# Kernel optimization log

Measured on AMD Instinct MI355X. Metric: run time of the kernel, lower is better.

## Reference

```python
import jax, jax.numpy as jnp
import numpy as np

E, K = 8, 2            # num_experts, top_k
H, DFF = 1024, 2048    # embd_dim, d_ff
B, S = 4, 1024


def setup_inputs() -> dict:
    key = jax.random.key(0)
    ks = jax.random.split(key, 5)
    s_in = 1.0 / np.sqrt(H)
    s_ff = 1.0 / np.sqrt(DFF)
    return {
        "x": jax.random.normal(ks[0], (B, S, H), jnp.float32),
        "centroids": jax.random.normal(ks[1], (E, H), jnp.float32),
        # nn.Linear weights are [out, in]
        "gate_w": jax.random.normal(ks[2], (E, DFF, H), jnp.float32) * s_in,
        "up_w": jax.random.normal(ks[3], (E, DFF, H), jnp.float32) * s_in,
        "down_w": jax.random.normal(ks[4], (E, H, DFF), jnp.float32) * s_ff,
        "routing_bias": jnp.zeros((E,), jnp.float32),
    }


def reference(x, centroids, gate_w, up_w, down_w, routing_bias):
    Bb, Ss, Hh = x.shape
    xf = x.reshape(-1, Hh)  # [T, H]
    # sigmoid affinity router + (non-trainable) routing bias
    affinity = jax.nn.sigmoid(xf @ centroids.T)          # [T, E]
    topk_scores, topk_idx = jax.lax.top_k(affinity + routing_bias, K)  # [T, K]
    topk_w = jax.nn.softmax(topk_scores, axis=-1)        # [T, K]

    # Dense per-expert SwiGLU FFN on all tokens (same math as the
    # sort/gather grouped loop; selection happens in the gather below).
    g = jnp.einsum('th,efh->etf', xf, gate_w)            # [E, T, DFF]
    u = jnp.einsum('th,efh->etf', xf, up_w)              # [E, T, DFF]
    y = jnp.einsum('etf,ehf->eth', jax.nn.silu(g) * u, down_w)  # [E, T, H]

    yt = jnp.transpose(y, (1, 0, 2))                     # [T, E, H]
    sel = jnp.take_along_axis(yt, topk_idx[:, :, None], axis=1)  # [T, K, H]
    out_flat = jnp.sum(sel * topk_w[:, :, None], axis=1)  # [T, H]

    counts = jnp.bincount(topk_idx.ravel(), length=E)    # per-expert token counts
    return out_flat.reshape(Bb, Ss, Hh), counts
```

## Files before the change

### kernel.cpp

```cpp
#include <hip/hip_runtime.h>
#include <math.h>

constexpr int E = 8, H = 1024, DFF = 2048, T = 4096;
constexpr int TR = 8192;
constexpr int MAXJ = 72;

typedef __bf16 bf16x8 __attribute__((ext_vector_type(8)));
typedef __bf16 bf16x4 __attribute__((ext_vector_type(4)));
typedef float f32x4 __attribute__((ext_vector_type(4)));

__device__ __forceinline__ void gload16(const void* g, void* l) {
    __builtin_amdgcn_global_load_lds(
        (const __attribute__((address_space(1))) unsigned int*)g,
        (__attribute__((address_space(3))) unsigned int*)l, 16, 0, 0);
}

__global__ __launch_bounds__(256) void k1_affinity(
    const float* __restrict__ x, const float* __restrict__ cent,
    const float* __restrict__ bias,
    int* __restrict__ se, float* __restrict__ sw) {
    __shared__ float cs[E * H];
    int tid = threadIdx.x;
    for (int i = tid; i < E * H / 4; i += 256)
        ((float4*)cs)[i] = ((const float4*)cent)[i];
    __syncthreads();

    int wave = tid >> 6, lane = tid & 63;
    int t = blockIdx.x * 4 + wave;
    const float4* xr = (const float4*)(x + (size_t)t * H);
    float acc[E] = {};
    #pragma unroll
    for (int it = 0; it < 4; it++) {
        float4 xv = xr[lane + it * 64];
        #pragma unroll
        for (int e = 0; e < E; e++) {
            float4 cv = ((const float4*)(cs + e * H))[lane + it * 64];
            acc[e] = fmaf(xv.x, cv.x, acc[e]);
            acc[e] = fmaf(xv.y, cv.y, acc[e]);
            acc[e] = fmaf(xv.z, cv.z, acc[e]);
            acc[e] = fmaf(xv.w, cv.w, acc[e]);
        }
    }
    #pragma unroll
    for (int off = 32; off; off >>= 1)
        #pragma unroll
        for (int e = 0; e < E; e++) acc[e] += __shfl_down(acc[e], off);

    if (lane == 0) {
        float s[E];
        #pragma unroll
        for (int e = 0; e < E; e++)
            s[e] = 1.0f / (1.0f + expf(-acc[e])) + bias[e];
        int i0 = 0;
        for (int e = 1; e < E; e++) if (s[e] > s[i0]) i0 = e;
        int i1 = -1;
        for (int e = 0; e < E; e++) {
            if (e == i0) continue;
            if (i1 < 0 || s[e] > s[i1]) i1 = e;
        }
        float m = fmaxf(s[i0], s[i1]);
        float w0 = expf(s[i0] - m), w1 = expf(s[i1] - m);
        float inv = 1.0f / (w0 + w1);
        se[2 * t] = i0;     sw[2 * t] = w0 * inv;
        se[2 * t + 1] = i1; sw[2 * t + 1] = w1 * inv;
    }
}

__global__ __launch_bounds__(256) void k1b_partition(
    const int* __restrict__ se, int* __restrict__ token_list,
    int* __restrict__ sp, int* __restrict__ cnt) {
    int e = blockIdx.x;
    int tid = threadIdx.x;
    int wave = tid >> 6, lane = tid & 63;
    __shared__ int wsum[4];
    int running = 0;
    for (int c0 = 0; c0 < 2 * T; c0 += 256) {
        int i = c0 + tid;
        bool pred = (se[i] == e);
        unsigned long long mask = __ballot(pred);
        int pos_in_wave = __popcll(mask & ((1ull << lane) - 1ull));
        if (lane == 0) wsum[wave] = __popcll(mask);
        __syncthreads();
        int wbase = 0;
        for (int w2 = 0; w2 < wave; w2++) wbase += wsum[w2];
        int total = wsum[0] + wsum[1] + wsum[2] + wsum[3];
        if (pred) {
            int p = running + wbase + pos_in_wave;
            token_list[e * T + p] = i >> 1;
            sp[i] = p;
        }
        running += total;
        __syncthreads();
    }
    if (tid == 0) cnt[e] = running;
}

__global__ void k15_offsets(const int* __restrict__ cnt, int* __restrict__ off,
                            float* __restrict__ out_counts,
                            int* __restrict__ jobs, int* __restrict__ njobs) {
    if (threadIdx.x == 0) {
        int acc = 0, nj = 0;
        for (int e = 0; e < E; e++) {
            off[e] = acc; acc += cnt[e];
            int mts = (cnt[e] + 127) >> 7;
            for (int mt = 0; mt < mts; mt++) jobs[nj++] = e * 64 + mt;
        }
        njobs[0] = nj;
    }
    if (threadIdx.x < E) out_counts[threadIdx.x] = (float)cnt[threadIdx.x];
}

__global__ __launch_bounds__(256) void k_conv(const float* __restrict__ in,
                                              __bf16* __restrict__ out, int n4) {
    int i = blockIdx.x * 256 + threadIdx.x;
    if (i < n4) {
        float4 v = ((const float4*)in)[i];
        bf16x4 o = {(__bf16)v.x, (__bf16)v.y, (__bf16)v.z, (__bf16)v.w};
        ((bf16x4*)out)[i] = o;
    }
}

__global__ __launch_bounds__(256) void k_conv3(
    const float* __restrict__ gw, __bf16* __restrict__ gwb,
    const float* __restrict__ uw, __bf16* __restrict__ uwb,
    const float* __restrict__ x, __bf16* __restrict__ xb,
    int w4, int x4) {
    int i = blockIdx.x * 256 + threadIdx.x;
    const float* in; __bf16* out; int idx;
    if (i < w4) { in = gw; out = gwb; idx = i; }
    else if (i < 2 * w4) { in = uw; out = uwb; idx = i - w4; }
    else { idx = i - 2 * w4; if (idx >= x4) return; in = x; out = xb; }
    float4 v = ((const float4*)in)[idx];
    bf16x4 o = {(__bf16)v.x, (__bf16)v.y, (__bf16)v.z, (__bf16)v.w};
    ((bf16x4*)out)[idx] = o;
}

__global__ __launch_bounds__(256, 2) void k2_gateup(
    const __bf16* __restrict__ xb, const __bf16* __restrict__ gwb,
    const __bf16* __restrict__ uwb, const int* __restrict__ cnt,
    const int* __restrict__ off, const int* __restrict__ token_list,
    const int* __restrict__ jobs, const int* __restrict__ njobs,
    __bf16* __restrict__ h) {
    int jt = blockIdx.x >> 4, nt = blockIdx.x & 15;
    if (jt >= njobs[0]) return;
    int job = jobs[jt];
    int e = job >> 6, mt = job & 63;
    int Me = cnt[e], offe = off[e];

    __shared__ __bf16 As[128 * 64];
    __shared__ __bf16 Bg[128 * 64];
    __shared__ __bf16 Bu[128 * 64];

    int tid = threadIdx.x;
    int lane = tid & 63, w = tid >> 6;
    int wm = w >> 1, wn = w & 1;

    const __bf16* asrc[4];
    const __bf16 *bsg[4], *bsu[4];
    #pragma unroll
    for (int rr = 0; rr < 4; rr++) {
        int l = rr * 256 + tid;
        int row = l >> 3, sl = l & 7;
        int gr = mt * 128 + row; if (gr >= Me) gr = Me - 1;
        int tok = token_list[e * T + gr];
        asrc[rr] = xb + (size_t)tok * H + ((sl ^ (row & 7)) * 8);
        size_t base = ((size_t)e * DFF + nt * 128 + row) * H + ((sl ^ (row & 7)) * 8);
        bsg[rr] = gwb + base;
        bsu[rr] = uwb + base;
    }

    f32x4 accg[4][4] = {};
    f32x4 accu[4][4] = {};
    int kq = lane >> 4, m15 = lane & 15;

    for (int k0 = 0; k0 < H; k0 += 64) {
        #pragma unroll
        for (int rr = 0; rr < 4; rr++) {
            gload16(asrc[rr] + k0, &As[(rr * 256 + tid) * 8]);
            gload16(bsg[rr] + k0, &Bg[(rr * 256 + tid) * 8]);
            gload16(bsu[rr] + k0, &Bu[(rr * 256 + tid) * 8]);
        }
        __syncthreads();

        #pragma unroll
        for (int kc = 0; kc < 2; kc++) {
            bf16x8 af[4], gf[4], uf[4];
            #pragma unroll
            for (int i = 0; i < 4; i++) {
                int row = wm * 64 + i * 16 + m15;
                int sl = (kc * 4 + kq) ^ (row & 7);
                af[i] = *(const bf16x8*)&As[row * 64 + sl * 8];
            }
            #pragma unroll
            for (int j = 0; j < 4; j++) {
                int row = wn * 64 + j * 16 + m15;
                int sl = (kc * 4 + kq) ^ (row & 7);
                gf[j] = *(const bf16x8*)&Bg[row * 64 + sl * 8];
                uf[j] = *(const bf16x8*)&Bu[row * 64 + sl * 8];
            }
            #pragma unroll
            for (int i = 0; i < 4; i++)
                #pragma unroll
                for (int j = 0; j < 4; j++) {
                    accg[i][j] = __builtin_amdgcn_mfma_f32_16x16x32_bf16(af[i], gf[j], accg[i][j], 0, 0, 0);
                    accu[i][j] = __builtin_amdgcn_mfma_f32_16x16x32_bf16(af[i], uf[j], accu[i][j], 0, 0, 0);
                }
        }
        __syncthreads();
    }

    #pragma unroll
    for (int i = 0; i < 4; i++)
        #pragma unroll
        for (int j = 0; j < 4; j++) {
            int nloc = wn * 64 + j * 16 + m15;
            size_t c = (size_t)nt * 128 + nloc;
            #pragma unroll
            for (int p = 0; p < 4; p++) {
                int mloc = wm * 64 + i * 16 + kq * 4 + p;
                int mrow = mt * 128 + mloc;
                if (mrow < Me) {
                    float g = accg[i][j][p], u = accu[i][j][p];
                    float sig = 1.0f / (1.0f + __expf(-g));
                    h[(size_t)(offe + mrow) * DFF + c] = (__bf16)(g * sig * u);
                }
            }
        }
}

__global__ __launch_bounds__(512, 2) void k3_down(
    const __bf16* __restrict__ h, const __bf16* __restrict__ dwb,
    const int* __restrict__ cnt, const int* __restrict__ off,
    const int* __restrict__ jobs, const int* __restrict__ njobs,
    __bf16* __restrict__ y) {
    int jt = blockIdx.x >> 2, nt = blockIdx.x & 3;
    if (jt >= njobs[0]) return;
    int job = jobs[jt];
    int e = job >> 6, mt = job & 63;
    int Me = cnt[e], offe = off[e];

    __shared__ __bf16 As[128 * 64];
    __shared__ __bf16 Bs[256 * 64];

    int tid = threadIdx.x;
    int lane = tid & 63, w = tid >> 6;
    int wm = w >> 2, wn = w & 3;

    const __bf16* asrc[2];
    #pragma unroll
    for (int rr = 0; rr < 2; rr++) {
        int l = rr * 512 + tid;
        int row = l >> 3, sl = l & 7;
        int koff = (sl ^ (row & 7)) * 8;
        int gr = mt * 128 + row; if (gr >= Me) gr = Me - 1;
        asrc[rr] = h + (size_t)(offe + gr) * DFF + koff;
    }
    const __bf16* bsrc[4];
    #pragma unroll
    for (int rr = 0; rr < 4; rr++) {
        int l = rr * 512 + tid;
        int row = l >> 3, sl = l & 7;
        int koff = (sl ^ (row & 7)) * 8;
        bsrc[rr] = dwb + ((size_t)e * H + nt * 256 + row) * DFF + koff;
    }

    f32x4 acc[4][4] = {};
    int kq = lane >> 4, m15 = lane & 15;

    for (int k0 = 0; k0 < DFF; k0 += 64) {
        #pragma unroll
        for (int rr = 0; rr < 2; rr++)
            gload16(asrc[rr] + k0, &As[(rr * 512 + tid) * 8]);
        #pragma unroll
        for (int rr = 0; rr < 4; rr++)
            gload16(bsrc[rr] + k0, &Bs[(rr * 512 + tid) * 8]);
        __syncthreads();

        #pragma unroll
        for (int kc = 0; kc < 2; kc++) {
            bf16x8 af[4], bf[4];
            #pragma unroll
            for (int i = 0; i < 4; i++) {
                int row = wm * 64 + i * 16 + m15;
                int sl = (kc * 4 + kq) ^ (row & 7);
                af[i] = *(const bf16x8*)&As[row * 64 + sl * 8];
            }
            #pragma unroll
            for (int j = 0; j < 4; j++) {
                int row = wn * 64 + j * 16 + m15;
                int sl = (kc * 4 + kq) ^ (row & 7);
                bf[j] = *(const bf16x8*)&Bs[row * 64 + sl * 8];
            }
            #pragma unroll
            for (int i = 0; i < 4; i++)
                #pragma unroll
                for (int j = 0; j < 4; j++)
                    acc[i][j] = __builtin_amdgcn_mfma_f32_16x16x32_bf16(af[i], bf[j], acc[i][j], 0, 0, 0);
        }
        __syncthreads();
    }

    #pragma unroll
    for (int i = 0; i < 4; i++)
        #pragma unroll
        for (int j = 0; j < 4; j++) {
            int nglob = nt * 256 + wn * 64 + j * 16 + m15;
            #pragma unroll
            for (int p = 0; p < 4; p++) {
                int mloc = wm * 64 + i * 16 + kq * 4 + p;
                int mrow = mt * 128 + mloc;
                if (mrow < Me)
                    y[(size_t)(offe + mrow) * H + nglob] = (__bf16)acc[i][j][p];
            }
        }
}

__global__ __launch_bounds__(256) void k_gather(
    const __bf16* __restrict__ y, const int* __restrict__ se,
    const int* __restrict__ sp, const float* __restrict__ sw,
    const int* __restrict__ off, float* __restrict__ out) {
    int t = blockIdx.x;
    int r0 = off[se[2 * t]] + sp[2 * t];
    int r1 = off[se[2 * t + 1]] + sp[2 * t + 1];
    float w0 = sw[2 * t], w1 = sw[2 * t + 1];
    const bf16x4* y0 = (const bf16x4*)(y + (size_t)r0 * H);
    const bf16x4* y1 = (const bf16x4*)(y + (size_t)r1 * H);
    float4* o = (float4*)(out + (size_t)t * H);
    int c = threadIdx.x;
    bf16x4 a = y0[c], b = y1[c];
    float4 v;
    v.x = w0 * (float)a[0] + w1 * (float)b[0];
    v.y = w0 * (float)a[1] + w1 * (float)b[1];
    v.z = w0 * (float)a[2] + w1 * (float)b[2];
    v.w = w0 * (float)a[3] + w1 * (float)b[3];
    o[c] = v;
}

extern "C" void kernel_launch(void* const* d_in, const int* in_sizes, int n_in,
                              void* d_out, int out_size, void* d_ws, size_t ws_size,
                              hipStream_t stream) {
    const float* x    = (const float*)d_in[0];
    const float* cent = (const float*)d_in[1];
    const float* gw   = (const float*)d_in[2];
    const float* uw   = (const float*)d_in[3];
    const float* dw   = (const float*)d_in[4];
    const float* bias = (const float*)d_in[5];
    float* out = (float*)d_out;

    char* ws = (char*)d_ws;
    int*   cnt        = (int*)(ws + 0);
    int*   off        = (int*)(ws + 64);
    int*   se         = (int*)(ws + 128);
    int*   sp         = (int*)(ws + 128 + 32768);
    float* sw         = (float*)(ws + 128 + 65536);
    int*   token_list = (int*)(ws + 128 + 98304);
    int*   jobs       = (int*)(ws + 229504);
    int*   njobs      = (int*)(ws + 229824);
    const size_t MB = 1u << 20;
    __bf16* gwb = (__bf16*)(ws + 1 * MB);
    __bf16* uwb = (__bf16*)(ws + 1 * MB + 33554432);
    __bf16* dwb = gwb;
    __bf16* y   = uwb;
    __bf16* xb  = (__bf16*)(ws + 1 * MB + 67108864);
    __bf16* h   = (__bf16*)(ws + 1 * MB + 75497472);

    const int W4 = E * DFF * H / 4;
    const int X4 = T * H / 4;
    const int C3 = 2 * W4 + X4;

    k_conv3<<<(C3 + 255) / 256, 256, 0, stream>>>(gw, gwb, uw, uwb, x, xb, W4, X4);
    k1_affinity<<<T / 4, 256, 0, stream>>>(x, cent, bias, se, sw);
    k1b_partition<<<E, 256, 0, stream>>>(se, token_list, sp, cnt);
    k15_offsets<<<1, 64, 0, stream>>>(cnt, off, out + (size_t)T * H, jobs, njobs);
    k2_gateup<<<MAXJ * 16, 256, 0, stream>>>(xb, gwb, uwb, cnt, off, token_list, jobs, njobs, h);
    k_conv<<<(W4 + 255) / 256, 256, 0, stream>>>(dw, dwb, W4);
    k3_down<<<MAXJ * 4, 512, 0, stream>>>(h, dwb, cnt, off, jobs, njobs, y);
    k_gather<<<T, 256, 0, stream>>>(y, se, sp, sw, off, out);
}
```

Before: 389.4 us.

## Fuse weighted combine into down-proj via atomics and fold x conversion into router

The down-projection epilogue now scales each row by its routing weight and atomically adds it into the zero-initialised fp32 output, which removes the intermediate y buffer and the separate gather kernel. The bf16 conversion of x moves into the affinity kernel, and the partition kernel stores per-row weights instead of slot positions. Launch-bound occupancy hints are raised for both GEMMs. In exchange it adds a memset of the output, scattered fp32 atomics that make the summation order nondeterministic, and possible register pressure from the higher occupancy targets.

```diff
diff --git a/kernel.cpp b/kernel.cpp
--- a/kernel.cpp
+++ b/kernel.cpp
@@ -18,7 +18,7 @@
 __global__ __launch_bounds__(256) void k1_affinity(
     const float* __restrict__ x, const float* __restrict__ cent,
     const float* __restrict__ bias,
-    int* __restrict__ se, float* __restrict__ sw) {
+    int* __restrict__ se, float* __restrict__ sw, __bf16* __restrict__ xb) {
     __shared__ float cs[E * H];
     int tid = threadIdx.x;
     for (int i = tid; i < E * H / 4; i += 256)
@@ -28,10 +28,13 @@
     int wave = tid >> 6, lane = tid & 63;
     int t = blockIdx.x * 4 + wave;
     const float4* xr = (const float4*)(x + (size_t)t * H);
+    bf16x4* xw = (bf16x4*)(xb + (size_t)t * H);
     float acc[E] = {};
     #pragma unroll
     for (int it = 0; it < 4; it++) {
         float4 xv = xr[lane + it * 64];
+        bf16x4 o = {(__bf16)xv.x, (__bf16)xv.y, (__bf16)xv.z, (__bf16)xv.w};
+        xw[lane + it * 64] = o;
         #pragma unroll
         for (int e = 0; e < E; e++) {
             float4 cv = ((const float4*)(cs + e * H))[lane + it * 64];
@@ -67,8 +70,9 @@
 }
 
 __global__ __launch_bounds__(256) void k1b_partition(
-    const int* __restrict__ se, int* __restrict__ token_list,
-    int* __restrict__ sp, int* __restrict__ cnt) {
+    const int* __restrict__ se, const float* __restrict__ sw,
+    int* __restrict__ token_list, float* __restrict__ roww,
+    int* __restrict__ cnt) {
     int e = blockIdx.x;
     int tid = threadIdx.x;
     int wave = tid >> 6, lane = tid & 63;
@@ -87,7 +91,7 @@
         if (pred) {
             int p = running + wbase + pos_in_wave;
             token_list[e * T + p] = i >> 1;
-            sp[i] = p;
+            roww[e * T + p] = sw[i];
         }
         running += total;
         __syncthreads();
@@ -120,22 +124,19 @@
     }
 }
 
-__global__ __launch_bounds__(256) void k_conv3(
+__global__ __launch_bounds__(256) void k_conv2(
     const float* __restrict__ gw, __bf16* __restrict__ gwb,
-    const float* __restrict__ uw, __bf16* __restrict__ uwb,
-    const float* __restrict__ x, __bf16* __restrict__ xb,
-    int w4, int x4) {
+    const float* __restrict__ uw, __bf16* __restrict__ uwb, int w4) {
     int i = blockIdx.x * 256 + threadIdx.x;
     const float* in; __bf16* out; int idx;
     if (i < w4) { in = gw; out = gwb; idx = i; }
-    else if (i < 2 * w4) { in = uw; out = uwb; idx = i - w4; }
-    else { idx = i - 2 * w4; if (idx >= x4) return; in = x; out = xb; }
+    else { idx = i - w4; if (idx >= w4) return; in = uw; out = uwb; }
     float4 v = ((const float4*)in)[idx];
     bf16x4 o = {(__bf16)v.x, (__bf16)v.y, (__bf16)v.z, (__bf16)v.w};
     ((bf16x4*)out)[idx] = o;
 }
 
-__global__ __launch_bounds__(256, 2) void k2_gateup(
+__global__ __launch_bounds__(256, 3) void k2_gateup(
     const __bf16* __restrict__ xb, const __bf16* __restrict__ gwb,
     const __bf16* __restrict__ uwb, const int* __restrict__ cnt,
     const int* __restrict__ off, const int* __restrict__ token_list,
@@ -228,11 +229,12 @@
         }
 }
 
-__global__ __launch_bounds__(512, 2) void k3_down(
+__global__ __launch_bounds__(512, 4) void k3_down(
     const __bf16* __restrict__ h, const __bf16* __restrict__ dwb,
     const int* __restrict__ cnt, const int* __restrict__ off,
+    const int* __restrict__ token_list, const float* __restrict__ roww,
     const int* __restrict__ jobs, const int* __restrict__ njobs,
-    __bf16* __restrict__ y) {
+    float* __restrict__ out) {
     int jt = blockIdx.x >> 2, nt = blockIdx.x & 3;
     if (jt >= njobs[0]) return;
     int job = jobs[jt];
@@ -301,39 +303,22 @@
     }
 
     #pragma unroll
-    for (int i = 0; i < 4; i++)
-        #pragma unroll
-        for (int j = 0; j < 4; j++) {
-            int nglob = nt * 256 + wn * 64 + j * 16 + m15;
-            #pragma unroll
-            for (int p = 0; p < 4; p++) {
-                int mloc = wm * 64 + i * 16 + kq * 4 + p;
-                int mrow = mt * 128 + mloc;
-                if (mrow < Me)
-                    y[(size_t)(offe + mrow) * H + nglob] = (__bf16)acc[i][j][p];
-            }
-        }
-}
-
-__global__ __launch_bounds__(256) void k_gather(
-    const __bf16* __restrict__ y, const int* __restrict__ se,
-    const int* __restrict__ sp, const float* __restrict__ sw,
-    const int* __restrict__ off, float* __restrict__ out) {
-    int t = blockIdx.x;
-    int r0 = off[se[2 * t]] + sp[2 * t];
-    int r1 = off[se[2 * t + 1]] + sp[2 * t + 1];
-    float w0 = sw[2 * t], w1 = sw[2 * t + 1];
-    const bf16x4* y0 = (const bf16x4*)(y + (size_t)r0 * H);
-    const bf16x4* y1 = (const bf16x4*)(y + (size_t)r1 * H);
-    float4* o = (float4*)(out + (size_t)t * H);
-    int c = threadIdx.x;
-    bf16x4 a = y0[c], b = y1[c];
-    float4 v;
-    v.x = w0 * (float)a[0] + w1 * (float)b[0];
-    v.y = w0 * (float)a[1] + w1 * (float)b[1];
-    v.z = w0 * (float)a[2] + w1 * (float)b[2];
-    v.w = w0 * (float)a[3] + w1 * (float)b[3];
-    o[c] = v;
+    for (int i = 0; i < 4; i++) {
+        int mbase = mt * 128 + wm * 64 + i * 16 + kq * 4;
+        #pragma unroll
+        for (int p = 0; p < 4; p++) {
+            int mrow = mbase + p;
+            if (mrow >= Me) continue;
+            int tok = token_list[e * T + mrow];
+            float wgt = roww[e * T + mrow];
+            float* orow = out + (size_t)tok * H;
+            #pragma unroll
+            for (int j = 0; j < 4; j++) {
+                int nglob = nt * 256 + wn * 64 + j * 16 + m15;
+                atomicAdd(&orow[nglob], wgt * acc[i][j][p]);
+            }
+        }
+    }
 }
 
 extern "C" void kernel_launch(void* const* d_in, const int* in_sizes, int n_in,
@@ -351,29 +336,26 @@
     int*   cnt        = (int*)(ws + 0);
     int*   off        = (int*)(ws + 64);
     int*   se         = (int*)(ws + 128);
-    int*   sp         = (int*)(ws + 128 + 32768);
-    float* sw         = (float*)(ws + 128 + 65536);
-    int*   token_list = (int*)(ws + 128 + 98304);
-    int*   jobs       = (int*)(ws + 229504);
-    int*   njobs      = (int*)(ws + 229824);
+    float* sw         = (float*)(ws + 32896);
+    int*   token_list = (int*)(ws + 65664);
+    float* roww       = (float*)(ws + 196736);
+    int*   jobs       = (int*)(ws + 327808);
+    int*   njobs      = (int*)(ws + 328128);
     const size_t MB = 1u << 20;
     __bf16* gwb = (__bf16*)(ws + 1 * MB);
     __bf16* uwb = (__bf16*)(ws + 1 * MB + 33554432);
-    __bf16* dwb = gwb;
-    __bf16* y   = uwb;
+    __bf16* dwb = uwb;
     __bf16* xb  = (__bf16*)(ws + 1 * MB + 67108864);
     __bf16* h   = (__bf16*)(ws + 1 * MB + 75497472);
 
     const int W4 = E * DFF * H / 4;
-    const int X4 = T * H / 4;
-    const int C3 = 2 * W4 + X4;
-
-    k_conv3<<<(C3 + 255) / 256, 256, 0, stream>>>(gw, gwb, uw, uwb, x, xb, W4, X4);
-    k1_affinity<<<T / 4, 256, 0, stream>>>(x, cent, bias, se, sw);
-    k1b_partition<<<E, 256, 0, stream>>>(se, token_list, sp, cnt);
+
+    hipMemsetAsync(out, 0, (size_t)T * H * sizeof(float), stream);
+    k_conv2<<<(2 * W4 + 255) / 256, 256, 0, stream>>>(gw, gwb, uw, uwb, W4);
+    k1_affinity<<<T / 4, 256, 0, stream>>>(x, cent, bias, se, sw, xb);
+    k1b_partition<<<E, 256, 0, stream>>>(se, sw, token_list, roww, cnt);
     k15_offsets<<<1, 64, 0, stream>>>(cnt, off, out + (size_t)T * H, jobs, njobs);
     k2_gateup<<<MAXJ * 16, 256, 0, stream>>>(xb, gwb, uwb, cnt, off, token_list, jobs, njobs, h);
     k_conv<<<(W4 + 255) / 256, 256, 0, stream>>>(dw, dwb, W4);
-    k3_down<<<MAXJ * 4, 512, 0, stream>>>(h, dwb, cnt, off, jobs, njobs, y);
-    k_gather<<<T, 256, 0, stream>>>(y, se, sp, sw, off, out);
-}
+    k3_down<<<MAXJ * 4, 512, 0, stream>>>(h, dwb, cnt, off, token_list, roww, jobs, njobs, out);
+}
```

New measurement: 580.4 us. 1.49x slower.
